# Optimization experiments

Hardware: AMD Instinct MI355X
Metric: run time of the kernel (lower is better)

## Reference

```python
import jax, jax.numpy as jnp
import numpy as np

SCORE_THRESHOLD = 0.15
IOU_THRESHOLD = 0.5
MAX_OUTPUT = 10          # tf.image.non_max_suppression(..., 10, ...)
NUM_CLASSES = 80
NUM_ANCHORS = 5
NEG = -1e9               # score for suppressed / below-threshold boxes


def setup_inputs() -> dict:
    key = jax.random.key(0)
    k1, k2 = jax.random.split(key)
    preds = jax.random.normal(k1, (16, 52, 52, NUM_ANCHORS * (5 + NUM_CLASSES)), dtype=jnp.float32)
    # anchor priors in grid-cell units, typical YOLOv2 range
    anchors = jax.random.uniform(k2, (NUM_ANCHORS, 2), dtype=jnp.float32, minval=0.5, maxval=6.0)
    return {"preds": preds, "anchors": anchors}


def _decode(preds, anchors):
    """YOLOv2 head decode (the `_interpret_prediction` callable)."""
    B, H, W, _ = preds.shape
    A = anchors.shape[0]
    p = preds.reshape(B, H, W, A, 5 + NUM_CLASSES)
    gy, gx = jnp.meshgrid(jnp.arange(H, dtype=preds.dtype),
                          jnp.arange(W, dtype=preds.dtype), indexing="ij")
    grid = jnp.stack([gx, gy], axis=-1)[None, :, :, None, :]   # (1,H,W,1,2) in (x,y)
    dims = jnp.array([W, H], dtype=preds.dtype)
    box_xy = (jax.nn.sigmoid(p[..., :2]) + grid) / dims        # normalized centers
    box_wh = jnp.exp(p[..., 2:4]) * anchors[None, None, None, :, :] / dims
    box_confidence = jax.nn.sigmoid(p[..., 4:5])
    box_class_probs = jax.nn.softmax(p[..., 5:], axis=-1)
    return box_xy, box_wh, box_confidence, box_class_probs


def _iou(box, boxes):
    """IoU of one box (ymin,xmin,ymax,xmax) against all boxes [N,4]."""
    tl = jnp.maximum(box[:2], boxes[:, :2])
    br = jnp.minimum(box[2:], boxes[:, 2:])
    inter = jnp.prod(jnp.maximum(br - tl, 0.0), axis=-1)
    area1 = jnp.prod(jnp.maximum(box[2:] - box[:2], 0.0))
    area2 = jnp.prod(jnp.maximum(boxes[:, 2:] - boxes[:, :2], 0.0), axis=-1)
    return inter / (area1 + area2 - inter + 1e-9)


def reference(preds, anchors):
    box_xy, box_wh, box_confidence, box_class_probs = _decode(preds, anchors)
    box_mins = box_xy - box_wh / 2.0
    box_maxes = box_xy + box_wh / 2.0
    # (ymin, xmin, ymax, xmax), matching the K.concatenate in the source
    boxes = jnp.concatenate([box_mins[..., 1:2], box_mins[..., 0:1],
                             box_maxes[..., 1:2], box_maxes[..., 0:1]], axis=-1)
    box_scores = box_confidence * box_class_probs
    box_classes = jnp.argmax(box_scores, axis=-1)
    box_class_scores = jnp.max(box_scores, axis=-1)

    boxes = boxes.reshape(-1, 4)                       # [N,4]
    scores = box_class_scores.reshape(-1)              # [N]
    classes = box_classes.reshape(-1).astype(preds.dtype)

    # score-threshold mask: instead of boolean_mask (dynamic shape), kill scores
    live = jnp.where(scores >= SCORE_THRESHOLD, scores, NEG)

    # greedy NMS, fixed MAX_OUTPUT iterations (semantics of tf.image.non_max_suppression)
    def step(cur_scores, _):
        i = jnp.argmax(cur_scores)
        s = cur_scores[i]
        valid = s > NEG / 2
        box = boxes[i]
        ious = _iou(box, boxes)
        nxt = jnp.where(ious > IOU_THRESHOLD, NEG, cur_scores).at[i].set(NEG)
        row = jnp.where(valid,
                        jnp.concatenate([box, s[None], classes[i][None]]),
                        jnp.zeros((6,), dtype=preds.dtype))
        return nxt, row

    _, rows = jax.lax.scan(step, live, None, length=MAX_OUTPUT)
    return rows  # [10, 6] = (ymin, xmin, ymax, xmax, score, class); zero rows = padding
```

## Files before the change

kernel.cpp:

```cpp
#include <hip/hip_runtime.h>
#include <math.h>

#define A_N      5
#define GRID_HW  52
#define NCLS     80
#define CH       85
#define SCORE_T  0.15f
#define IOU_T    0.5f
#define NEGV     (-1e9f)
#define MAXOUT   10

#define BPB          64
#define DEC_THREADS  256
#define TILE_FLOATS  (BPB * CH)
#define TILE_F4      (TILE_FLOATS / 4)

#define NMS_THREADS  1024
#define NMS_LBOX     8192
#define KA           (NMS_LBOX / NMS_THREADS)

__global__ __launch_bounds__(DEC_THREADS) void decode_kernel(
    const float* __restrict__ preds,
    const float* __restrict__ anchors,
    float4* __restrict__ pbox, float* __restrict__ pscore,
    float* __restrict__ pcls,
    int* __restrict__ counter, int N, int capacity)
{
    __shared__ __align__(16) float lds[TILE_FLOATS];

    const int tile = blockIdx.x;
    const long long tile_f4_base = (long long)tile * TILE_F4;
    const long long total_f4 = ((long long)N * CH) / 4;
    const float4* src = (const float4*)preds;
    float4* dst = (float4*)lds;

#pragma unroll
    for (int k = 0; k < (TILE_F4 + DEC_THREADS - 1) / DEC_THREADS; ++k) {
        int idx = (int)threadIdx.x + k * DEC_THREADS;
        if (idx < TILE_F4 && (tile_f4_base + idx) < total_f4)
            dst[idx] = src[tile_f4_base + idx];
    }
    __syncthreads();

    const int b = (int)threadIdx.x >> 2;
    const int q = (int)threadIdx.x & 3;
    const int gi = tile * BPB + b;
    const float* bp = lds + b * CH;
    const float* cl = bp + 5 + q * 20;

    float m = cl[0];
    int   am = q * 20;
#pragma unroll
    for (int j = 1; j < 20; ++j) {
        float x = cl[j];
        if (x > m) { m = x; am = q * 20 + j; }
    }
    float s = 0.0f;
#pragma unroll
    for (int j = 0; j < 20; ++j) s += expf(cl[j] - m);

#pragma unroll
    for (int off = 1; off <= 2; off <<= 1) {
        float m2 = __shfl_xor(m, off);
        float s2 = __shfl_xor(s, off);
        int   am2 = __shfl_xor(am, off);
        float M = fmaxf(m, m2);
        s = s * expf(m - M) + s2 * expf(m2 - M);
        if (m2 > m || (m2 == m && am2 < am)) am = am2;
        m = M;
    }

    if (q == 0 && gi < N) {
        float conf  = 1.0f / (1.0f + expf(-bp[4]));
        float score = conf / s;
        if (score >= SCORE_T) {
            int a = gi % A_N;
            int t = gi / A_N;
            int w = t % GRID_HW;
            int h = (t / GRID_HW) % GRID_HW;
            const float inv = 1.0f / (float)GRID_HW;
            float cx = (1.0f / (1.0f + expf(-bp[0])) + (float)w) * inv;
            float cy = (1.0f / (1.0f + expf(-bp[1])) + (float)h) * inv;
            float bw = expf(bp[2]) * anchors[2 * a]     * inv;
            float bh = expf(bp[3]) * anchors[2 * a + 1] * inv;

            int pos = atomicAdd(counter, 1);
            if (pos < capacity) {
                pbox[pos]   = make_float4(cy - 0.5f * bh, cx - 0.5f * bw,
                                          cy + 0.5f * bh, cx + 0.5f * bw);
                pscore[pos] = score;
                pcls[pos]   = (float)am;
            }
        }
    }
}

__global__ __launch_bounds__(NMS_THREADS) void nms_kernel(
    const float4* __restrict__ pbox, float* __restrict__ pscore,
    const float* __restrict__ pcls, const int* __restrict__ counter,
    int capacity, float* __restrict__ out)
{
    __shared__ __align__(16) float4 lbox[NMS_LBOX];
    __shared__ float psc[16];
    __shared__ int   pix[16];
    __shared__ int   swi;

    int M = *counter;
    if (M > capacity) M = capacity;
    const int tid  = (int)threadIdx.x;
    const int lane = tid & 63;
    const int wid  = tid >> 6;

    if (M <= NMS_LBOX) {
        float sc[KA];
#pragma unroll
        for (int k = 0; k < KA; ++k) {
            int j = tid + (k << 10);
            sc[k] = (j < M) ? pscore[j] : -INFINITY;
            if (j < M) lbox[j] = pbox[j];
        }
        __syncthreads();

        for (int it = 0; it < MAXOUT; ++it) {
            float bs = -INFINITY; int bi = -1;
#pragma unroll
            for (int k = 0; k < KA; ++k) {
                if (sc[k] > bs) { bs = sc[k]; bi = tid + (k << 10); }
            }
#pragma unroll
            for (int off = 32; off; off >>= 1) {
                float os = __shfl_xor(bs, off);
                int   oi = __shfl_xor(bi, off);
                if (os > bs || (os == bs && oi != -1 && (bi == -1 || oi < bi))) {
                    bs = os; bi = oi;
                }
            }
            if (lane == 0) { psc[wid] = bs; pix[wid] = bi; }
            __syncthreads();

            if (wid == 0 && lane < 16) {
                bs = psc[lane]; bi = pix[lane];
#pragma unroll
                for (int off = 8; off; off >>= 1) {
                    float os = __shfl_xor(bs, off);
                    int   oi = __shfl_xor(bi, off);
                    if (os > bs || (os == bs && oi != -1 && (bi == -1 || oi < bi))) {
                        bs = os; bi = oi;
                    }
                }
                if (lane == 0) {
                    bool valid = (bi >= 0) && (bs > NEGV * 0.5f);
                    swi = valid ? bi : -1;
                    if (valid) {
                        float4 b = lbox[bi];
                        out[it*6+0] = b.x; out[it*6+1] = b.y;
                        out[it*6+2] = b.z; out[it*6+3] = b.w;
                        out[it*6+4] = bs;  out[it*6+5] = pcls[bi];
                    } else {
                        out[it*6+0] = 0.f; out[it*6+1] = 0.f; out[it*6+2] = 0.f;
                        out[it*6+3] = 0.f; out[it*6+4] = 0.f; out[it*6+5] = 0.f;
                    }
                }
            }
            __syncthreads();

            int wi = swi;
            if (wi >= 0) {
                float4 wb = lbox[wi];
                float a1 = fmaxf(wb.z - wb.x, 0.f) * fmaxf(wb.w - wb.y, 0.f);
#pragma unroll
                for (int k = 0; k < KA; ++k) {
                    int j = tid + (k << 10);
                    if (j == wi) sc[k] = NEGV;
                    if (j < M) {
                        float4 bj = lbox[j];
                        float ty = fmaxf(wb.x, bj.x);
                        float tx = fmaxf(wb.y, bj.y);
                        float by = fminf(wb.z, bj.z);
                        float bx = fminf(wb.w, bj.w);
                        float inter = fmaxf(by - ty, 0.f) * fmaxf(bx - tx, 0.f);
                        float a2 = fmaxf(bj.z - bj.x, 0.f) * fmaxf(bj.w - bj.y, 0.f);
                        float iou = inter / (a1 + a2 - inter + 1e-9f);
                        if (iou > IOU_T) sc[k] = NEGV;
                    }
                }
            }
        }
    } else {
        for (int it = 0; it < MAXOUT; ++it) {
            float bs = -INFINITY; int bi = -1;
            for (int j = tid; j < M; j += NMS_THREADS) {
                float s = pscore[j];
                if (s > bs) { bs = s; bi = j; }
            }
#pragma unroll
            for (int off = 32; off; off >>= 1) {
                float os = __shfl_xor(bs, off);
                int   oi = __shfl_xor(bi, off);
                if (os > bs || (os == bs && oi != -1 && (bi == -1 || oi < bi))) {
                    bs = os; bi = oi;
                }
            }
            if (lane == 0) { psc[wid] = bs; pix[wid] = bi; }
            __syncthreads();
            if (wid == 0 && lane < 16) {
                bs = psc[lane]; bi = pix[lane];
#pragma unroll
                for (int off = 8; off; off >>= 1) {
                    float os = __shfl_xor(bs, off);
                    int   oi = __shfl_xor(bi, off);
                    if (os > bs || (os == bs && oi != -1 && (bi == -1 || oi < bi))) {
                        bs = os; bi = oi;
                    }
                }
                if (lane == 0) {
                    bool valid = (bi >= 0) && (bs > NEGV * 0.5f);
                    swi = valid ? bi : -1;
                    if (valid) {
                        float4 b = pbox[bi];
                        out[it*6+0] = b.x; out[it*6+1] = b.y;
                        out[it*6+2] = b.z; out[it*6+3] = b.w;
                        out[it*6+4] = bs;  out[it*6+5] = pcls[bi];
                        pscore[bi] = NEGV;
                    } else {
                        out[it*6+0] = 0.f; out[it*6+1] = 0.f; out[it*6+2] = 0.f;
                        out[it*6+3] = 0.f; out[it*6+4] = 0.f; out[it*6+5] = 0.f;
                    }
                }
            }
            __syncthreads();
            int wi = swi;
            if (wi >= 0) {
                float4 wb = pbox[wi];
                float a1 = fmaxf(wb.z - wb.x, 0.f) * fmaxf(wb.w - wb.y, 0.f);
                for (int j = tid; j < M; j += NMS_THREADS) {
                    float4 bj = pbox[j];
                    float ty = fmaxf(wb.x, bj.x);
                    float tx = fmaxf(wb.y, bj.y);
                    float by = fminf(wb.z, bj.z);
                    float bx = fminf(wb.w, bj.w);
                    float inter = fmaxf(by - ty, 0.f) * fmaxf(bx - tx, 0.f);
                    float a2 = fmaxf(bj.z - bj.x, 0.f) * fmaxf(bj.w - bj.y, 0.f);
                    float iou = inter / (a1 + a2 - inter + 1e-9f);
                    if (iou > IOU_T) pscore[j] = NEGV;
                }
            }
            __syncthreads();
        }
    }
}

extern "C" void kernel_launch(void* const* d_in, const int* in_sizes, int n_in,
                              void* d_out, int out_size, void* d_ws, size_t ws_size,
                              hipStream_t stream) {
    (void)n_in; (void)out_size;
    const float* preds   = (const float*)d_in[0];
    const float* anchors = (const float*)d_in[1];
    float* out = (float*)d_out;

    int N = in_sizes[0] / CH;

    char* ws = (char*)d_ws;
    int* counter = (int*)ws;
    size_t avail = (ws_size > 64) ? (ws_size - 64) : 0;
    long long cap = (long long)(avail / (sizeof(float4) + 2 * sizeof(float)));
    if (cap > N) cap = N;
    if (cap < 0) cap = 0;
    int capacity = (int)cap;

    float4* pbox  = (float4*)(ws + 64);
    float* pscore = (float*)(pbox + capacity);
    float* pcls   = pscore + capacity;

    hipMemsetAsync(counter, 0, sizeof(int), stream);

    int nTiles = (N + BPB - 1) / BPB;
    decode_kernel<<<nTiles, DEC_THREADS, 0, stream>>>(
        preds, anchors, pbox, pscore, pcls, counter, N, capacity);
    nms_kernel<<<1, NMS_THREADS, 0, stream>>>(
        pbox, pscore, pcls, counter, capacity, out);
}
```

Baseline: 66.89 us.

## Rework decode with direct global-to-LDS loads, wave-aggregated atomics, smaller NMS block

The decode kernel now uses one 64-lane wave per 32-box tile. It fills LDS with the global_load_lds builtin, gives each box two lanes instead of four, uses fast __expf, and batches output slot allocation with a ballot plus a single atomic per wave. NMS drops to 256 threads with a 4096-box SoA LDS capacity and a simpler final reduction. The memset is replaced by a tiny init kernel. This targets load latency, atomic contention and NMS sync overhead, but NMS falls back to the slow global path whenever more than 4096 boxes pass the threshold, and __expf loosens accuracy.

Measured after the change: 76.58 us. 1.14x slower.

```diff
diff --git a/kernel.cpp b/kernel.cpp
--- a/kernel.cpp
+++ b/kernel.cpp
@@ -10,16 +10,28 @@
 #define NEGV     (-1e9f)
 #define MAXOUT   10
 
-#define BPB          64
-#define DEC_THREADS  256
+#define BPB          32
 #define TILE_FLOATS  (BPB * CH)
-#define TILE_F4      (TILE_FLOATS / 4)
-
-#define NMS_THREADS  1024
-#define NMS_LBOX     8192
-#define KA           (NMS_LBOX / NMS_THREADS)
-
-__global__ __launch_bounds__(DEC_THREADS) void decode_kernel(
+#define FULL_LOADS   10
+#define TAIL_LANES   40
+
+#define NMS_THREADS  256
+#define NCAP         4096
+#define NKA          (NCAP / NMS_THREADS)
+
+__device__ __forceinline__ float fexp(float x) { return __expf(x); }
+
+__device__ __forceinline__ void gload_lds16(const float* g, float* l) {
+    __builtin_amdgcn_global_load_lds(
+        (const __attribute__((address_space(1))) unsigned int*)g,
+        (__attribute__((address_space(3))) unsigned int*)l, 16, 0, 0);
+}
+
+__global__ void init_counter_kernel(int* __restrict__ counter) {
+    *counter = 0;
+}
+
+__global__ __launch_bounds__(64) void decode_kernel(
     const float* __restrict__ preds,
     const float* __restrict__ anchors,
     float4* __restrict__ pbox, float* __restrict__ pscore,
@@ -29,62 +41,70 @@
     __shared__ __align__(16) float lds[TILE_FLOATS];
 
     const int tile = blockIdx.x;
-    const long long tile_f4_base = (long long)tile * TILE_F4;
-    const long long total_f4 = ((long long)N * CH) / 4;
-    const float4* src = (const float4*)preds;
-    float4* dst = (float4*)lds;
-
-#pragma unroll
-    for (int k = 0; k < (TILE_F4 + DEC_THREADS - 1) / DEC_THREADS; ++k) {
-        int idx = (int)threadIdx.x + k * DEC_THREADS;
-        if (idx < TILE_F4 && (tile_f4_base + idx) < total_f4)
-            dst[idx] = src[tile_f4_base + idx];
+    const int lane = (int)threadIdx.x;
+    const float* gbase = preds + (size_t)tile * TILE_FLOATS;
+
+#pragma unroll
+    for (int i = 0; i < FULL_LOADS; ++i) {
+        gload_lds16(gbase + (size_t)(i * 64 + lane) * 4, &lds[i * 256]);
+    }
+    if (lane < TAIL_LANES) {
+        gload_lds16(gbase + (size_t)(FULL_LOADS * 64 + lane) * 4,
+                    &lds[FULL_LOADS * 256]);
     }
     __syncthreads();
 
-    const int b = (int)threadIdx.x >> 2;
-    const int q = (int)threadIdx.x & 3;
+    const int b  = lane >> 1;
+    const int h  = lane & 1;
     const int gi = tile * BPB + b;
     const float* bp = lds + b * CH;
-    const float* cl = bp + 5 + q * 20;
+    const float* cl = bp + 5 + h * 40;
 
     float m = cl[0];
-    int   am = q * 20;
-#pragma unroll
-    for (int j = 1; j < 20; ++j) {
+    int   am = h * 40;
+#pragma unroll
+    for (int j = 1; j < 40; ++j) {
         float x = cl[j];
-        if (x > m) { m = x; am = q * 20 + j; }
+        if (x > m) { m = x; am = h * 40 + j; }
     }
     float s = 0.0f;
 #pragma unroll
-    for (int j = 0; j < 20; ++j) s += expf(cl[j] - m);
-
-#pragma unroll
-    for (int off = 1; off <= 2; off <<= 1) {
-        float m2 = __shfl_xor(m, off);
-        float s2 = __shfl_xor(s, off);
-        int   am2 = __shfl_xor(am, off);
+    for (int j = 0; j < 40; ++j) s += fexp(cl[j] - m);
+
+    {
+        float m2 = __shfl_xor(m, 1);
+        float s2 = __shfl_xor(s, 1);
+        int   am2 = __shfl_xor(am, 1);
         float M = fmaxf(m, m2);
-        s = s * expf(m - M) + s2 * expf(m2 - M);
+        s = s * fexp(m - M) + s2 * fexp(m2 - M);
         if (m2 > m || (m2 == m && am2 < am)) am = am2;
         m = M;
     }
 
-    if (q == 0 && gi < N) {
-        float conf  = 1.0f / (1.0f + expf(-bp[4]));
-        float score = conf / s;
-        if (score >= SCORE_T) {
+    float conf  = 1.0f / (1.0f + fexp(-bp[4]));
+    float score = conf / s;
+
+    bool live = (h == 0) && (gi < N) && (score >= SCORE_T);
+
+    unsigned long long mask = __ballot(live);
+    if (mask) {
+        int nlive  = __popcll(mask);
+        int leader = (int)__ffsll((long long)mask) - 1;
+        int base_ = 0;
+        if (lane == leader) base_ = atomicAdd(counter, nlive);
+        base_ = __shfl(base_, leader);
+        if (live) {
             int a = gi % A_N;
             int t = gi / A_N;
-            int w = t % GRID_HW;
-            int h = (t / GRID_HW) % GRID_HW;
+            int wx = t % GRID_HW;
+            int hy = (t / GRID_HW) % GRID_HW;
             const float inv = 1.0f / (float)GRID_HW;
-            float cx = (1.0f / (1.0f + expf(-bp[0])) + (float)w) * inv;
-            float cy = (1.0f / (1.0f + expf(-bp[1])) + (float)h) * inv;
-            float bw = expf(bp[2]) * anchors[2 * a]     * inv;
-            float bh = expf(bp[3]) * anchors[2 * a + 1] * inv;
-
-            int pos = atomicAdd(counter, 1);
+            float cx = (1.0f / (1.0f + fexp(-bp[0])) + (float)wx) * inv;
+            float cy = (1.0f / (1.0f + fexp(-bp[1])) + (float)hy) * inv;
+            float bw = fexp(bp[2]) * anchors[2 * a]     * inv;
+            float bh = fexp(bp[3]) * anchors[2 * a + 1] * inv;
+
+            int pos = base_ + __popcll(mask & ((1ull << lane) - 1));
             if (pos < capacity) {
                 pbox[pos]   = make_float4(cy - 0.5f * bh, cx - 0.5f * bw,
                                           cy + 0.5f * bh, cx + 0.5f * bw);
@@ -100,10 +120,9 @@
     const float* __restrict__ pcls, const int* __restrict__ counter,
     int capacity, float* __restrict__ out)
 {
-    __shared__ __align__(16) float4 lbox[NMS_LBOX];
-    __shared__ float psc[16];
-    __shared__ int   pix[16];
-    __shared__ int   swi;
+    __shared__ float sy0[NCAP], sx0[NCAP], sy1[NCAP], sx1[NCAP], ssc[NCAP];
+    __shared__ float psc[4];
+    __shared__ int   pix[4];
 
     int M = *counter;
     if (M > capacity) M = capacity;
@@ -111,21 +130,27 @@
     const int lane = tid & 63;
     const int wid  = tid >> 6;
 
-    if (M <= NMS_LBOX) {
-        float sc[KA];
-#pragma unroll
-        for (int k = 0; k < KA; ++k) {
-            int j = tid + (k << 10);
-            sc[k] = (j < M) ? pscore[j] : -INFINITY;
-            if (j < M) lbox[j] = pbox[j];
+    if (M <= NCAP) {
+#pragma unroll
+        for (int k = 0; k < NKA; ++k) {
+            int j = tid + (k << 8);
+            if (j < M) {
+                float4 bx = pbox[j];
+                sy0[j] = bx.x; sx0[j] = bx.y; sy1[j] = bx.z; sx1[j] = bx.w;
+                ssc[j] = pscore[j];
+            } else {
+                ssc[j] = -INFINITY;
+            }
         }
         __syncthreads();
 
         for (int it = 0; it < MAXOUT; ++it) {
             float bs = -INFINITY; int bi = -1;
 #pragma unroll
-            for (int k = 0; k < KA; ++k) {
-                if (sc[k] > bs) { bs = sc[k]; bi = tid + (k << 10); }
+            for (int k = 0; k < NKA; ++k) {
+                int j = tid + (k << 8);
+                float v = ssc[j];
+                if (v > bs) { bs = v; bi = j; }
             }
 #pragma unroll
             for (int off = 32; off; off >>= 1) {
@@ -138,60 +163,52 @@
             if (lane == 0) { psc[wid] = bs; pix[wid] = bi; }
             __syncthreads();
 
-            if (wid == 0 && lane < 16) {
-                bs = psc[lane]; bi = pix[lane];
-#pragma unroll
-                for (int off = 8; off; off >>= 1) {
-                    float os = __shfl_xor(bs, off);
-                    int   oi = __shfl_xor(bi, off);
-                    if (os > bs || (os == bs && oi != -1 && (bi == -1 || oi < bi))) {
-                        bs = os; bi = oi;
-                    }
-                }
-                if (lane == 0) {
-                    bool valid = (bi >= 0) && (bs > NEGV * 0.5f);
-                    swi = valid ? bi : -1;
-                    if (valid) {
-                        float4 b = lbox[bi];
-                        out[it*6+0] = b.x; out[it*6+1] = b.y;
-                        out[it*6+2] = b.z; out[it*6+3] = b.w;
-                        out[it*6+4] = bs;  out[it*6+5] = pcls[bi];
-                    } else {
-                        out[it*6+0] = 0.f; out[it*6+1] = 0.f; out[it*6+2] = 0.f;
-                        out[it*6+3] = 0.f; out[it*6+4] = 0.f; out[it*6+5] = 0.f;
-                    }
-                }
-            }
-            __syncthreads();
-
-            int wi = swi;
-            if (wi >= 0) {
-                float4 wb = lbox[wi];
-                float a1 = fmaxf(wb.z - wb.x, 0.f) * fmaxf(wb.w - wb.y, 0.f);
-#pragma unroll
-                for (int k = 0; k < KA; ++k) {
-                    int j = tid + (k << 10);
-                    if (j == wi) sc[k] = NEGV;
-                    if (j < M) {
-                        float4 bj = lbox[j];
-                        float ty = fmaxf(wb.x, bj.x);
-                        float tx = fmaxf(wb.y, bj.y);
-                        float by = fminf(wb.z, bj.z);
-                        float bx = fminf(wb.w, bj.w);
-                        float inter = fmaxf(by - ty, 0.f) * fmaxf(bx - tx, 0.f);
-                        float a2 = fmaxf(bj.z - bj.x, 0.f) * fmaxf(bj.w - bj.y, 0.f);
-                        float iou = inter / (a1 + a2 - inter + 1e-9f);
-                        if (iou > IOU_T) sc[k] = NEGV;
-                    }
-                }
-            }
+            bs = psc[0]; bi = pix[0];
+#pragma unroll
+            for (int w = 1; w < 4; ++w) {
+                float os = psc[w]; int oi = pix[w];
+                if (os > bs || (os == bs && oi != -1 && (bi == -1 || oi < bi))) {
+                    bs = os; bi = oi;
+                }
+            }
+            bool valid = (bi >= 0) && (bs > NEGV * 0.5f);
+
+            if (tid == 0) {
+                if (valid) {
+                    out[it*6+0] = sy0[bi]; out[it*6+1] = sx0[bi];
+                    out[it*6+2] = sy1[bi]; out[it*6+3] = sx1[bi];
+                    out[it*6+4] = bs;      out[it*6+5] = pcls[bi];
+                } else {
+                    out[it*6+0] = 0.f; out[it*6+1] = 0.f; out[it*6+2] = 0.f;
+                    out[it*6+3] = 0.f; out[it*6+4] = 0.f; out[it*6+5] = 0.f;
+                }
+            }
+
+            if (valid) {
+                float wy0 = sy0[bi], wx0 = sx0[bi], wy1 = sy1[bi], wx1 = sx1[bi];
+                float a1 = fmaxf(wy1 - wy0, 0.f) * fmaxf(wx1 - wx0, 0.f);
+#pragma unroll
+                for (int k = 0; k < NKA; ++k) {
+                    int j = tid + (k << 8);
+                    if (j == bi) ssc[j] = NEGV;
+                    float ty = fmaxf(wy0, sy0[j]);
+                    float tx = fmaxf(wx0, sx0[j]);
+                    float by = fminf(wy1, sy1[j]);
+                    float bx = fminf(wx1, sx1[j]);
+                    float inter = fmaxf(by - ty, 0.f) * fmaxf(bx - tx, 0.f);
+                    float a2 = fmaxf(sy1[j] - sy0[j], 0.f) * fmaxf(sx1[j] - sx0[j], 0.f);
+                    float iou = inter / (a1 + a2 - inter + 1e-9f);
+                    if (iou > IOU_T && j < M) ssc[j] = NEGV;
+                }
+            }
+            __syncthreads();
         }
     } else {
         for (int it = 0; it < MAXOUT; ++it) {
             float bs = -INFINITY; int bi = -1;
             for (int j = tid; j < M; j += NMS_THREADS) {
-                float s = pscore[j];
-                if (s > bs) { bs = s; bi = j; }
+                float v = pscore[j];
+                if (v > bs) { bs = v; bi = j; }
             }
 #pragma unroll
             for (int off = 32; off; off >>= 1) {
@@ -203,35 +220,30 @@
             }
             if (lane == 0) { psc[wid] = bs; pix[wid] = bi; }
             __syncthreads();
-            if (wid == 0 && lane < 16) {
-                bs = psc[lane]; bi = pix[lane];
-#pragma unroll
-                for (int off = 8; off; off >>= 1) {
-                    float os = __shfl_xor(bs, off);
-                    int   oi = __shfl_xor(bi, off);
-                    if (os > bs || (os == bs && oi != -1 && (bi == -1 || oi < bi))) {
-                        bs = os; bi = oi;
-                    }
-                }
-                if (lane == 0) {
-                    bool valid = (bi >= 0) && (bs > NEGV * 0.5f);
-                    swi = valid ? bi : -1;
-                    if (valid) {
-                        float4 b = pbox[bi];
-                        out[it*6+0] = b.x; out[it*6+1] = b.y;
-                        out[it*6+2] = b.z; out[it*6+3] = b.w;
-                        out[it*6+4] = bs;  out[it*6+5] = pcls[bi];
-                        pscore[bi] = NEGV;
-                    } else {
-                        out[it*6+0] = 0.f; out[it*6+1] = 0.f; out[it*6+2] = 0.f;
-                        out[it*6+3] = 0.f; out[it*6+4] = 0.f; out[it*6+5] = 0.f;
-                    }
-                }
-            }
-            __syncthreads();
-            int wi = swi;
-            if (wi >= 0) {
-                float4 wb = pbox[wi];
+            bs = psc[0]; bi = pix[0];
+#pragma unroll
+            for (int w = 1; w < 4; ++w) {
+                float os = psc[w]; int oi = pix[w];
+                if (os > bs || (os == bs && oi != -1 && (bi == -1 || oi < bi))) {
+                    bs = os; bi = oi;
+                }
+            }
+            bool valid = (bi >= 0) && (bs > NEGV * 0.5f);
+            if (tid == 0) {
+                if (valid) {
+                    float4 bx = pbox[bi];
+                    out[it*6+0] = bx.x; out[it*6+1] = bx.y;
+                    out[it*6+2] = bx.z; out[it*6+3] = bx.w;
+                    out[it*6+4] = bs;   out[it*6+5] = pcls[bi];
+                    pscore[bi] = NEGV;
+                } else {
+                    out[it*6+0] = 0.f; out[it*6+1] = 0.f; out[it*6+2] = 0.f;
+                    out[it*6+3] = 0.f; out[it*6+4] = 0.f; out[it*6+5] = 0.f;
+                }
+            }
+            __syncthreads();
+            if (valid) {
+                float4 wb = pbox[bi];
                 float a1 = fmaxf(wb.z - wb.x, 0.f) * fmaxf(wb.w - wb.y, 0.f);
                 for (int j = tid; j < M; j += NMS_THREADS) {
                     float4 bj = pbox[j];
@@ -272,10 +284,10 @@
     float* pscore = (float*)(pbox + capacity);
     float* pcls   = pscore + capacity;
 
-    hipMemsetAsync(counter, 0, sizeof(int), stream);
+    init_counter_kernel<<<1, 1, 0, stream>>>(counter);
 
     int nTiles = (N + BPB - 1) / BPB;
-    decode_kernel<<<nTiles, DEC_THREADS, 0, stream>>>(
+    decode_kernel<<<nTiles, 64, 0, stream>>>(
         preds, anchors, pbox, pscore, pcls, counter, N, capacity);
     nms_kernel<<<1, NMS_THREADS, 0, stream>>>(
         pbox, pscore, pcls, counter, capacity, out);
```
